# Kernel tuning notes

Hardware: AMD Instinct MI355X
Metric: run time of the kernel (lower is better)

## Reference

```python
import jax, jax.numpy as jnp
import numpy as np

BATCH, SEQ, HIDDEN = 2, 4096, 4096
HEADS, HEAD_DIM, BLOCK = 32, 128, 256
LAYER_IDX, N_LAYERS = 1, 32
EPS = 1e-5


def setup_inputs() -> dict:
    key = jax.random.key(0)
    ks = jax.random.split(key, 5)
    s = 0.02
    return {
        "hidden_states": jax.random.normal(ks[0], (BATCH, SEQ, HIDDEN), jnp.float32),
        "qkv_w": jax.random.normal(ks[1], (3 * HEADS * HEAD_DIM, HIDDEN), jnp.float32) * s,
        "out_w": jax.random.normal(ks[2], (HIDDEN, HEADS * HEAD_DIM), jnp.float32) * s,
        "gate_w": jax.random.normal(ks[3], (HEADS * HEAD_DIM, HIDDEN), jnp.float32) * s,
        "norm_w": jnp.ones((HEADS * HEAD_DIM,), jnp.float32),
    }


def _decays():
    # slope_rate: (h,1,1)
    base = 1.0 / 2.0 ** (8.0 / HEADS)
    exponent = jnp.arange(HEADS, dtype=jnp.float32) + 1.0
    factor = 1.0 - LAYER_IDX / (N_LAYERS - 1 + 1e-5) + 1e-5
    slope = (base ** exponent * factor)[:, None, None]
    r = jnp.arange(BLOCK, dtype=jnp.float32) + 1.0
    q_decay = jnp.exp(-slope * r[:, None])                 # (h, block, 1)
    k_decay = jnp.exp(-slope * (BLOCK - r)[:, None])       # (h, block, 1)
    diff = r[:, None] - r[None, :]                         # (block, block): i - j
    diag = slope[None] * diff[None, None]                  # (1, h, block, block)
    diag = jnp.where(diag >= 0, -diag, -jnp.inf)
    diag_decay = jnp.exp(diag)                             # causal intra-block decay
    block_decay = jnp.exp(-slope * BLOCK)                  # (h,1,1)
    return q_decay, k_decay, diag_decay, block_decay


def reference(hidden_states, qkv_w, out_w, gate_w, norm_w):
    b, s, _ = hidden_states.shape
    h, d, bs = HEADS, HEAD_DIM, BLOCK
    nb = s // bs
    q_decay, k_decay, diag_decay, block_decay = _decays()

    # qkv projection + silu, split per-head into q,k,v
    qkv = jax.nn.silu(hidden_states @ qkv_w.T)             # (b,s,3hd)
    qkv = qkv.reshape(b, s, h, 3, d)
    q = jnp.moveaxis(qkv[:, :, :, 0], 2, 1)                # (b,h,s,d)
    k = jnp.moveaxis(qkv[:, :, :, 1], 2, 1)
    v = jnp.moveaxis(qkv[:, :, :, 2], 2, 1)

    # split sequence into blocks, scan leading axis = block index
    def to_blocks(x):
        return jnp.moveaxis(x.reshape(b, h, nb, bs, d), 2, 0)  # (nb,b,h,bs,d)

    qb, kb, vb = to_blocks(q), to_blocks(k), to_blocks(v)

    def step(kv, blk):
        cq, ck, cv = blk
        # intra-block quadratic attention with causal decay
        scores = jnp.einsum('bhnd,bhmd->bhnm', cq, ck) * diag_decay
        intra = jnp.einsum('bhnm,bhmd->bhnd', scores, cv)
        # inter-block via decayed recurrent state kv: (b,h,d,d)
        inter = jnp.einsum('bhnd,bhde->bhne', cq * q_decay, kv)
        kv_next = kv * block_decay + jnp.einsum('bhnd,bhne->bhde', ck * k_decay, cv)
        return kv_next, intra + inter

    kv0 = jnp.zeros((b, h, d, d), hidden_states.dtype)
    _, out_blocks = jax.lax.scan(step, kv0, (qb, kb, vb))  # (nb,b,h,bs,d)

    attn = jnp.moveaxis(out_blocks, 0, 2)                  # (b,h,nb,bs,d)
    attn = attn.reshape(b, h, s, d).transpose(0, 2, 1, 3).reshape(b, s, h * d)

    # RMSNorm (fp32 accumulation, as MixtralRMSNorm)
    xf = attn.astype(jnp.float32)
    xf = xf * jax.lax.rsqrt(jnp.mean(xf * xf, axis=-1, keepdims=True) + EPS)
    normed = norm_w * xf.astype(attn.dtype)

    gate = jax.nn.sigmoid(hidden_states @ gate_w.T)
    return (gate * normed) @ out_w.T
```

## Files before the change

### kernel.cpp

```cpp
#include <hip/hip_runtime.h>

typedef unsigned short u16;
typedef __attribute__((ext_vector_type(4))) float f32x4;
typedef __attribute__((ext_vector_type(8))) __bf16 bf16x8;

#define SEQ   4096
#define HID   4096
#define HID3  12288

__device__ __forceinline__ float bf2f(u16 u){
  union { unsigned int i; float f; } v; v.i = ((unsigned int)u) << 16; return v.f;
}
__device__ __forceinline__ u16 f2bf(float f){
  union { float f; unsigned int i; } v; v.f = f;
  unsigned int r = (v.i + 0x7FFFu + ((v.i >> 16) & 1u)) >> 16;
  return (u16)r;
}
__device__ __forceinline__ float slope_of(int h){
  const float factor = 1.0f - 1.0f/(31.0f + 1e-5f) + 1e-5f;
  return exp2f(-0.25f * (float)(h + 1)) * factor;
}
__device__ __forceinline__ bf16x8 ld_bf8(const u16* p){
  return __builtin_bit_cast(bf16x8, *(const uint4*)p);
}
__device__ __forceinline__ void gload_lds16(const u16* g, u16* l){
  __builtin_amdgcn_global_load_lds((const __attribute__((address_space(1))) void*)g,
                                   (__attribute__((address_space(3))) void*)l, 16, 0, 0);
}

__global__ __launch_bounds__(256) void cvt4p_kernel(const float* __restrict__ s0,
                                                    const float* __restrict__ s1,
                                                    const float* __restrict__ s2,
                                                    const float* __restrict__ s3,
                                                    u16* __restrict__ dst){
  int c = blockIdx.x;
  int tr = c >> 7, kch = c & 127;
  const float* src; int rowbase;
  if (tr < 32){ src = s0; rowbase = tr * 256; }
  else if (tr < 80){ src = s1; rowbase = (tr - 32) * 256; }
  else if (tr < 96){ src = s2; rowbase = (tr - 80) * 256; }
  else { src = s3; rowbase = (tr - 96) * 256; }
  u16* out = dst + (long)c * 8192;
#pragma unroll
  for (int pass = 0; pass < 4; ++pass){
    int q = pass * 256 + threadIdx.x;
    int dr = q >> 3, up = q & 7;
    int ul = up ^ (dr & 7);
    int row = 2 * dr + (ul >> 2);
    int k8 = ul & 3;
    const float* sp = src + (long)(rowbase + row) * 4096 + kch * 32 + k8 * 8;
    float4 v0 = *(const float4*)sp;
    float4 v1 = *(const float4*)(sp + 4);
    ushort4 o0 = { f2bf(v0.x), f2bf(v0.y), f2bf(v0.z), f2bf(v0.w) };
    ushort4 o1 = { f2bf(v1.x), f2bf(v1.y), f2bf(v1.z), f2bf(v1.w) };
    *(ushort4*)(out + q * 8) = o0;
    *(ushort4*)(out + q * 8 + 4) = o1;
  }
}

template<int EPI>
__global__ __launch_bounds__(512) void gemm256(
    const u16* __restrict__ A, const u16* __restrict__ B, void* __restrict__ C,
    const u16* __restrict__ Aux, const float* __restrict__ Rs,
    const float* __restrict__ Nw, int M, int N, int K)
{
  __shared__ u16 ring[5][16384];
  const int t = threadIdx.x;
  const int w = t >> 6, l = t & 63, lr = l & 15, lk = l >> 4;
  const int mw = w >> 2, nw = w & 3;
  const int nbn = N >> 8;
  const int nkc = K >> 5;
  int nwg = gridDim.x;
  int bid = blockIdx.x;
  int bswz = (bid & 7) * (nwg >> 3) + (bid >> 3);
  int bm = bswz / nbn, bn = bswz % nbn;
  const int NT = K >> 6;

  int offA[8], offB[4];
#pragma unroll
  for (int fn = 0; fn < 8; ++fn){
    int row = mw * 128 + fn * 16 + lr;
    offA[fn] = (row >> 1) * 64 + (((((row & 1) << 2) + lk) ^ ((row >> 1) & 7)) << 3);
  }
#pragma unroll
  for (int fe = 0; fe < 4; ++fe){
    int row = nw * 64 + fe * 16 + lr;
    offB[fe] = (row >> 1) * 64 + (((((row & 1) << 2) + lk) ^ ((row >> 1) & 7)) << 3);
  }

  auto stageA = [&](int kt, int c, int slot, int i){
    gload_lds16(A + ((long)bm * nkc + kt * 2 + c) * 8192 + i * 4096 + t * 8,
                &ring[slot][i * 4096 + w * 512]);
  };
  auto stageB = [&](int kt, int c, int slot, int i){
    gload_lds16(B + ((long)bn * nkc + kt * 2 + c) * 8192 + i * 4096 + t * 8,
                &ring[slot][8192 + i * 4096 + w * 512]);
  };

  f32x4 acc[8][4] = {};

  stageA(0,0,0,0); stageA(0,0,0,1); stageB(0,0,0,0); stageB(0,0,0,1);
  stageA(0,1,1,0); stageA(0,1,1,1); stageB(0,1,1,0); stageB(0,1,1,1);
  if (1 < NT){ stageA(1,0,2,0); stageA(1,0,2,1); stageB(1,0,2,0); stageB(1,0,2,1); }
  asm volatile("s_waitcnt vmcnt(4)" ::: "memory");
  __builtin_amdgcn_s_barrier();

  int sa = 0;
  for (int p = 0; p < NT; ++p){
    int sb = sa + 1; if (sb >= 5) sb -= 5;
    int sx = sa + 3; if (sx >= 5) sx -= 5;
    int sy = sa + 4; if (sy >= 5) sy -= 5;
    const u16* Aa = &ring[sa][0];
    const u16* Ab = &ring[sb][0];
    const u16* Ba = &ring[sa][8192];
    const u16* Bb = &ring[sb][8192];
    bf16x8 bh0[4], bh1[4], afc0[8], afc1[8];

#pragma unroll
    for (int fe = 0; fe < 4; ++fe) bh0[fe] = ld_bf8(Ba + offB[fe]);
#pragma unroll
    for (int fn = 0; fn < 4; ++fn) afc0[fn] = ld_bf8(Aa + offA[fn]);
#pragma unroll
    for (int fn = 4; fn < 8; ++fn) afc0[fn] = ld_bf8(Aa + offA[fn]);
    if (p + 1 < NT){ stageA(p+1, 1, sx, 0); stageA(p+1, 1, sx, 1); }
    asm volatile("s_waitcnt lgkmcnt(4)" ::: "memory");
    __builtin_amdgcn_sched_barrier(0);
    __builtin_amdgcn_s_setprio(1);
#pragma unroll
    for (int fn = 0; fn < 4; ++fn)
#pragma unroll
      for (int fe = 0; fe < 4; ++fe)
        acc[fn][fe] = __builtin_amdgcn_mfma_f32_16x16x32_bf16(afc0[fn], bh0[fe], acc[fn][fe], 0, 0, 0);
    __builtin_amdgcn_s_setprio(0);

#pragma unroll
    for (int fe = 0; fe < 4; ++fe) bh1[fe] = ld_bf8(Bb + offB[fe]);
#pragma unroll
    for (int fn = 0; fn < 4; ++fn) afc1[fn] = ld_bf8(Ab + offA[fn]);
    if (p + 1 < NT){ stageB(p+1, 1, sx, 0); stageB(p+1, 1, sx, 1); }
    asm volatile("s_waitcnt lgkmcnt(8)" ::: "memory");
    __builtin_amdgcn_sched_barrier(0);
    __builtin_amdgcn_s_setprio(1);
#pragma unroll
    for (int fn = 4; fn < 8; ++fn)
#pragma unroll
      for (int fe = 0; fe < 4; ++fe)
        acc[fn][fe] = __builtin_amdgcn_mfma_f32_16x16x32_bf16(afc0[fn], bh0[fe], acc[fn][fe], 0, 0, 0);
    __builtin_amdgcn_s_setprio(0);

#pragma unroll
    for (int fn = 4; fn < 8; ++fn) afc1[fn] = ld_bf8(Ab + offA[fn]);
    if (p + 2 < NT){ stageA(p+2, 0, sy, 0); stageA(p+2, 0, sy, 1); }
    asm volatile("s_waitcnt lgkmcnt(4)" ::: "memory");
    __builtin_amdgcn_sched_barrier(0);
    __builtin_amdgcn_s_setprio(1);
#pragma unroll
    for (int fn = 0; fn < 4; ++fn)
#pragma unroll
      for (int fe = 0; fe < 4; ++fe)
        acc[fn][fe] = __builtin_amdgcn_mfma_f32_16x16x32_bf16(afc1[fn], bh1[fe], acc[fn][fe], 0, 0, 0);
    __builtin_amdgcn_s_setprio(0);

    if (p + 2 < NT){ stageB(p+2, 0, sy, 0); stageB(p+2, 0, sy, 1); }
    asm volatile("s_waitcnt lgkmcnt(0)" ::: "memory");
    __builtin_amdgcn_sched_barrier(0);
    __builtin_amdgcn_s_setprio(1);
#pragma unroll
    for (int fn = 4; fn < 8; ++fn)
#pragma unroll
      for (int fe = 0; fe < 4; ++fe)
        acc[fn][fe] = __builtin_amdgcn_mfma_f32_16x16x32_bf16(afc1[fn], bh1[fe], acc[fn][fe], 0, 0, 0);
    __builtin_amdgcn_s_setprio(0);

    if (p + 2 < NT) asm volatile("s_waitcnt vmcnt(4)" ::: "memory");
    else            asm volatile("s_waitcnt vmcnt(0)" ::: "memory");
    __builtin_amdgcn_s_barrier();
    sa += 2; if (sa >= 5) sa -= 5;
  }

  long crow = (long)bm * 256 + mw * 128 + lk * 4;
  long ccol = (long)bn * 256 + nw * 64 + lr;
#pragma unroll
  for (int fn = 0; fn < 8; ++fn)
#pragma unroll
    for (int fe = 0; fe < 4; ++fe)
#pragma unroll
      for (int reg = 0; reg < 4; ++reg){
        long row = crow + fn * 16 + reg;
        long col = ccol + fe * 16;
        float x = acc[fn][fe][reg];
        if (EPI == 0){
          ((u16*)C)[row * N + col] = f2bf(x / (1.0f + __expf(-x)));
        } else if (EPI == 1){
          float g = 1.0f / (1.0f + __expf(-x));
          float a = bf2f(Aux[row * N + col]);
          int r256 = (int)row & 255;
          int dr2 = r256 >> 1;
          int ul2 = ((r256 & 1) << 2) | (((int)col & 31) >> 3);
          int u2 = ul2 ^ (dr2 & 7);
          long idx = ((long)(row >> 8) * 128 + (col >> 5)) * 8192 + dr2 * 64 + u2 * 8 + (col & 7);
          ((u16*)C)[idx] = f2bf(g * a * Rs[row] * Nw[col]);
        } else {
          ((float*)C)[row * N + col] = x;
        }
      }
}

__global__ __launch_bounds__(256) void attn_contrib(
    const u16* __restrict__ qkv, float* __restrict__ ct)
{
  __shared__ u16 VT[128 * 258];
  __shared__ u16 KT[128 * 258];
  int wg = blockIdx.x;
  int bh = wg >> 4, blk = wg & 15;
  int b = bh >> 5, h = bh & 31;
  int t = threadIdx.x;
  float slope = slope_of(h);
  const u16* kg = qkv + ((long)(b * SEQ + blk * 256)) * HID3 + h * 384 + 128;
  const u16* vg = kg + 128;
#pragma unroll
  for (int i = 0; i < 16; ++i){
    int chunk = t + i * 256;
    int row = chunk >> 4, c8 = (chunk & 15) << 3;
    float kd = __expf(-slope * (float)(255 - row));
    uint4 kk = *(const uint4*)&kg[(long)row * HID3 + c8];
    uint4 vv = *(const uint4*)&vg[(long)row * HID3 + c8];
    const u16* ks = (const u16*)&kk;
    const u16* vs = (const u16*)&vv;
#pragma unroll
    for (int x = 0; x < 8; ++x){
      KT[(c8 + x) * 258 + row] = f2bf(bf2f(ks[x]) * kd);
      VT[(c8 + x) * 258 + row] = vs[x];
    }
  }
  __syncthreads();
  int w = t >> 6, l = t & 63, lr = l & 15, lk = l >> 4;
  int we = (w >> 1) * 64, wd = (w & 1) * 64;
  f32x4 acc[4][4] = {};
  for (int nc = 0; nc < 8; ++nc){
    bf16x8 va[4], kb[4];
#pragma unroll
    for (int f = 0; f < 4; ++f) va[f] = ld_bf8(&VT[(we + f * 16 + lr) * 258 + nc * 32 + lk * 8]);
#pragma unroll
    for (int f = 0; f < 4; ++f) kb[f] = ld_bf8(&KT[(wd + f * 16 + lr) * 258 + nc * 32 + lk * 8]);
#pragma unroll
    for (int fe = 0; fe < 4; ++fe)
#pragma unroll
      for (int fd = 0; fd < 4; ++fd)
        acc[fe][fd] = __builtin_amdgcn_mfma_f32_16x16x32_bf16(va[fe], kb[fd], acc[fe][fd], 0, 0, 0);
  }
  float* out = ct + (long)wg * 16384;
#pragma unroll
  for (int fe = 0; fe < 4; ++fe)
#pragma unroll
    for (int fd = 0; fd < 4; ++fd)
#pragma unroll
      for (int reg = 0; reg < 4; ++reg){
        int e = we + fe * 16 + lk * 4 + reg;
        int d = wd + fd * 16 + lr;
        out[e * 128 + d] = acc[fe][fd][reg];
      }
}

__global__ __launch_bounds__(256) void attn_scan(const float* __restrict__ ct,
                                                 u16* __restrict__ stTb)
{
  int g = blockIdx.x;
  int bh = g >> 2, sl = g & 3;
  int t = threadIdx.x;
  float bdec = __expf(-slope_of(bh & 31) * 256.0f);
  float cur[16];
#pragma unroll
  for (int i = 0; i < 16; ++i) cur[i] = 0.f;
  const float* base = ct + (long)bh * 16 * 16384 + sl * 4096;
  u16* ob = stTb + (long)bh * 16 * 16384 + sl * 4096;
  for (int blkI = 0; blkI < 16; ++blkI){
    const float* p = base + (long)blkI * 16384;
    u16* o = ob + (long)blkI * 16384;
#pragma unroll
    for (int i = 0; i < 16; ++i){
      o[t + i * 256] = f2bf(cur[i]);
      cur[i] = cur[i] * bdec + p[t + i * 256];
    }
  }
}

__global__ __launch_bounds__(512) void attn_mfma(
    const u16* __restrict__ qkv, const u16* __restrict__ stTb, u16* __restrict__ attn)
{
  __shared__ u16 Ks[256 * 130];
  __shared__ u16 VTs[128 * 258];
  __shared__ u16 Ps[4][64 * 34];
  int wg = blockIdx.x;
  int bh = wg >> 4, blk = wg & 15;
  int b = bh >> 5, h = bh & 31;
  int t = threadIdx.x;
  int w = t >> 6, l = t & 63, lr = l & 15, lk = l >> 4;
  int r = w >> 1, c = w & 1;
  float slope = slope_of(h);
  const u16* qg = qkv + ((long)(b * SEQ + blk * 256)) * HID3 + h * 384;
  const u16* kg = qg + 128;
  const u16* vg = qg + 256;

#pragma unroll
  for (int i = 0; i < 8; ++i){
    int chunk = t + i * 512;
    int row = chunk >> 4, c8 = (chunk & 15) << 3;
    *(uint4*)&Ks[row * 130 + c8] = *(const uint4*)&kg[(long)row * HID3 + c8];
    uint4 vv = *(const uint4*)&vg[(long)row * HID3 + c8];
    const u16* vs = (const u16*)&vv;
#pragma unroll
    for (int x = 0; x < 8; ++x) VTs[(c8 + x) * 258 + row] = vs[x];
  }
  bf16x8 qa[4][4];
#pragma unroll
  for (int fn = 0; fn < 4; ++fn)
#pragma unroll
    for (int kc = 0; kc < 4; ++kc)
      qa[fn][kc] = ld_bf8(&qg[(long)(r * 64 + fn * 16 + lr) * HID3 + kc * 32 + lk * 8]);
  f32x4 acc[4][4] = {};
  __syncthreads();

  int mtmax = 2 * r + 1;
  for (int mt = 0; mt < 8; ++mt){
    if (mt <= mtmax){
      f32x4 S[4] = {};
      int mrow = mt * 32 + c * 16 + lr;
      bf16x8 kb[4];
#pragma unroll
      for (int kc = 0; kc < 4; ++kc)
        kb[kc] = ld_bf8(&Ks[mrow * 130 + kc * 32 + lk * 8]);
#pragma unroll
      for (int fn = 0; fn < 4; ++fn)
#pragma unroll
        for (int kc = 0; kc < 4; ++kc)
          S[fn] = __builtin_amdgcn_mfma_f32_16x16x32_bf16(qa[fn][kc], kb[kc], S[fn], 0, 0, 0);
      int m = mt * 32 + c * 16 + lr;
#pragma unroll
      for (int fn = 0; fn < 4; ++fn)
#pragma unroll
        for (int reg = 0; reg < 4; ++reg){
          int n = r * 64 + fn * 16 + lk * 4 + reg;
          float dv = (n >= m) ? __expf(-slope * (float)(n - m)) : 0.f;
          Ps[r][(fn * 16 + lk * 4 + reg) * 34 + c * 16 + lr] = f2bf(S[fn][reg] * dv);
        }
    }
    __syncthreads();
    if (mt <= mtmax){
      bf16x8 pa[4], vb[4];
#pragma unroll
      for (int fn = 0; fn < 4; ++fn)
        pa[fn] = ld_bf8(&Ps[r][(fn * 16 + lr) * 34 + lk * 8]);
#pragma unroll
      for (int fe = 0; fe < 4; ++fe)
        vb[fe] = ld_bf8(&VTs[(c * 64 + fe * 16 + lr) * 258 + mt * 32 + lk * 8]);
#pragma unroll
      for (int fn = 0; fn < 4; ++fn)
#pragma unroll
        for (int fe = 0; fe < 4; ++fe)
          acc[fn][fe] = __builtin_amdgcn_mfma_f32_16x16x32_bf16(pa[fn], vb[fe], acc[fn][fe], 0, 0, 0);
    }
    __syncthreads();
  }

#pragma unroll
  for (int fn = 0; fn < 4; ++fn){
    int n = r * 64 + fn * 16 + lr;
    float qd = __expf(-slope * (float)(n + 1));
#pragma unroll
    for (int kc = 0; kc < 4; ++kc){
      union { bf16x8 v; u16 u[8]; } uu; uu.v = qa[fn][kc];
#pragma unroll
      for (int x = 0; x < 8; ++x) uu.u[x] = f2bf(bf2f(uu.u[x]) * qd);
      qa[fn][kc] = uu.v;
    }
  }
  const u16* sg = stTb + (long)(bh * 16 + blk) * 16384;
#pragma unroll
  for (int kc = 0; kc < 4; ++kc){
    bf16x8 sb2[4];
#pragma unroll
    for (int fe = 0; fe < 4; ++fe)
      sb2[fe] = ld_bf8(&sg[(c * 64 + fe * 16 + lr) * 128 + kc * 32 + lk * 8]);
#pragma unroll
    for (int fn = 0; fn < 4; ++fn)
#pragma unroll
      for (int fe = 0; fe < 4; ++fe)
        acc[fn][fe] = __builtin_amdgcn_mfma_f32_16x16x32_bf16(qa[fn][kc], sb2[fe], acc[fn][fe], 0, 0, 0);
  }

  u16* arow = attn + ((long)(b * SEQ + blk * 256)) * HID + h * 128;
#pragma unroll
  for (int fn = 0; fn < 4; ++fn)
#pragma unroll
    for (int fe = 0; fe < 4; ++fe)
#pragma unroll
      for (int reg = 0; reg < 4; ++reg){
        int n = r * 64 + fn * 16 + lk * 4 + reg;
        int col = c * 64 + fe * 16 + lr;
        arow[(long)n * HID + col] = f2bf(acc[fn][fe][reg]);
      }
}

__global__ __launch_bounds__(256) void rmsnorm_stats(const u16* __restrict__ attn,
                                                     float* __restrict__ rs)
{
  __shared__ float wsum[4];
  int row = blockIdx.x, t = threadIdx.x;
  const u16* p = attn + (long)row * HID;
  uint4 v0 = *(const uint4*)&p[t * 8];
  uint4 v1 = *(const uint4*)&p[t * 8 + 2048];
  const u16* a0 = (const u16*)&v0;
  const u16* a1 = (const u16*)&v1;
  float ss = 0.f;
#pragma unroll
  for (int x = 0; x < 8; ++x){
    float f0 = bf2f(a0[x]), f1 = bf2f(a1[x]);
    ss += f0 * f0 + f1 * f1;
  }
#pragma unroll
  for (int off = 32; off > 0; off >>= 1) ss += __shfl_down(ss, off);
  if ((t & 63) == 0) wsum[t >> 6] = ss;
  __syncthreads();
  if (t == 0)
    rs[row] = rsqrtf((wsum[0] + wsum[1] + wsum[2] + wsum[3]) * (1.0f / 4096.0f) + 1e-5f);
}

extern "C" void kernel_launch(void* const* d_in, const int* in_sizes, int n_in,
                              void* d_out, int out_size, void* d_ws, size_t ws_size,
                              hipStream_t stream)
{
  const float* hidden = (const float*)d_in[0];
  const float* qkv_w  = (const float*)d_in[1];
  const float* out_w  = (const float*)d_in[2];
  const float* gate_w = (const float*)d_in[3];
  const float* norm_w = (const float*)d_in[4];
  char* ws = (char*)d_ws;
  const long SZ_X  = 67108864L;
  const long SZ_WQ = 100663296L;
  const long SZ_WG = 33554432L;
  const long SZ_WO = 33554432L;
  const long SZ_QA = 201326592L;
  const long SZ_AT = 67108864L;
  u16* Xb   = (u16*)(ws);
  u16* Wq   = (u16*)(ws + SZ_X);
  u16* Wg   = (u16*)(ws + SZ_X + SZ_WQ);
  u16* Wo   = (u16*)(ws + SZ_X + SZ_WQ + SZ_WG);
  u16* qact = (u16*)(ws + SZ_X + SZ_WQ + SZ_WG + SZ_WO);
  u16* attn = (u16*)(ws + SZ_X + SZ_WQ + SZ_WG + SZ_WO + SZ_QA);
  float* st   = (float*)Wq;
  u16*   stTb = (u16*)(ws + SZ_X + 67108864L);
  float* rsbuf = (float*)Wq;
  u16* gated = qact;
  if (ws_size < (size_t)(SZ_X + SZ_WQ + SZ_WG + SZ_WO + SZ_QA + SZ_AT)) return;

  cvt4p_kernel<<<14336, 256, 0, stream>>>(hidden, qkv_w, gate_w, out_w, Xb);

  gemm256<0><<<32 * 48, 512, 0, stream>>>(Xb, Wq, (void*)qact, nullptr, nullptr, nullptr,
                                          8192, 12288, 4096);

  attn_contrib<<<1024, 256, 0, stream>>>(qact, st);
  attn_scan<<<256, 256, 0, stream>>>(st, stTb);
  attn_mfma<<<1024, 512, 0, stream>>>(qact, stTb, attn);
  rmsnorm_stats<<<8192, 256, 0, stream>>>(attn, rsbuf);

  gemm256<1><<<32 * 16, 512, 0, stream>>>(Xb, Wg, (void*)gated, attn, rsbuf, norm_w,
                                          8192, 4096, 4096);
  gemm256<2><<<32 * 16, 512, 0, stream>>>(gated, Wo, d_out, nullptr, nullptr, nullptr,
                                          8192, 4096, 4096);
}
```

Measured before the change: 1.529 ms.

## Load GEMM B operand directly from global into double-buffered registers, skipping LDS

The B tile is no longer staged through the shared-memory ring. Each wave now loads its B fragments straight from the pre-packed global layout into two register buffers, which alternate between even and odd iterations. This halves LDS use, which could allow a second workgroup per CU, and removes the LDS writes and reads for B. In exchange it raises register pressure, repeats B global reads across the waves that share a column slice, and relies on the vmcnt accounting and an even iteration count staying correct.

```diff
diff --git a/kernel.cpp b/kernel.cpp
--- a/kernel.cpp
+++ b/kernel.cpp
@@ -64,7 +64,7 @@
     const u16* __restrict__ Aux, const float* __restrict__ Rs,
     const float* __restrict__ Nw, int M, int N, int K)
 {
-  __shared__ u16 ring[5][16384];
+  __shared__ u16 ring[5][8192];
   const int t = threadIdx.x;
   const int w = t >> 6, l = t & 63, lr = l & 15, lk = l >> 4;
   const int mw = w >> 2, nw = w & 3;
@@ -92,36 +92,38 @@
     gload_lds16(A + ((long)bm * nkc + kt * 2 + c) * 8192 + i * 4096 + t * 8,
                 &ring[slot][i * 4096 + w * 512]);
   };
-  auto stageB = [&](int kt, int c, int slot, int i){
-    gload_lds16(B + ((long)bn * nkc + kt * 2 + c) * 8192 + i * 4096 + t * 8,
-                &ring[slot][8192 + i * 4096 + w * 512]);
+  const u16* Bt = B + (long)bn * nkc * 8192;
+  auto loadB = [&](int kt, bf16x8 (&dst)[4][2]){
+#pragma unroll
+    for (int c = 0; c < 2; ++c){
+      const u16* bc = Bt + ((long)kt * 2 + c) * 8192;
+#pragma unroll
+      for (int fe = 0; fe < 4; ++fe) dst[fe][c] = ld_bf8(bc + offB[fe]);
+    }
   };
 
   f32x4 acc[8][4] = {};
-
-  stageA(0,0,0,0); stageA(0,0,0,1); stageB(0,0,0,0); stageB(0,0,0,1);
-  stageA(0,1,1,0); stageA(0,1,1,1); stageB(0,1,1,0); stageB(0,1,1,1);
-  if (1 < NT){ stageA(1,0,2,0); stageA(1,0,2,1); stageB(1,0,2,0); stageB(1,0,2,1); }
-  asm volatile("s_waitcnt vmcnt(4)" ::: "memory");
+  bf16x8 bX[4][2], bY[4][2];
+
+  loadB(0, bX);
+  stageA(0,0,0,0); stageA(0,0,0,1);
+  stageA(0,1,1,0); stageA(0,1,1,1);
+  stageA(1,0,2,0); stageA(1,0,2,1);
+  asm volatile("s_waitcnt vmcnt(2)" ::: "memory");
   __builtin_amdgcn_s_barrier();
 
   int sa = 0;
-  for (int p = 0; p < NT; ++p){
+  auto period = [&](int p, bf16x8 (&bcur)[4][2], bf16x8 (&bnext)[4][2]){
     int sb = sa + 1; if (sb >= 5) sb -= 5;
     int sx = sa + 3; if (sx >= 5) sx -= 5;
     int sy = sa + 4; if (sy >= 5) sy -= 5;
     const u16* Aa = &ring[sa][0];
     const u16* Ab = &ring[sb][0];
-    const u16* Ba = &ring[sa][8192];
-    const u16* Bb = &ring[sb][8192];
-    bf16x8 bh0[4], bh1[4], afc0[8], afc1[8];
-
-#pragma unroll
-    for (int fe = 0; fe < 4; ++fe) bh0[fe] = ld_bf8(Ba + offB[fe]);
-#pragma unroll
-    for (int fn = 0; fn < 4; ++fn) afc0[fn] = ld_bf8(Aa + offA[fn]);
-#pragma unroll
-    for (int fn = 4; fn < 8; ++fn) afc0[fn] = ld_bf8(Aa + offA[fn]);
+    bf16x8 afc0[8], afc1[8];
+
+    if (p + 1 < NT) loadB(p + 1, bnext);
+#pragma unroll
+    for (int fn = 0; fn < 8; ++fn) afc0[fn] = ld_bf8(Aa + offA[fn]);
     if (p + 1 < NT){ stageA(p+1, 1, sx, 0); stageA(p+1, 1, sx, 1); }
     asm volatile("s_waitcnt lgkmcnt(4)" ::: "memory");
     __builtin_amdgcn_sched_barrier(0);
@@ -130,22 +132,19 @@
     for (int fn = 0; fn < 4; ++fn)
 #pragma unroll
       for (int fe = 0; fe < 4; ++fe)
-        acc[fn][fe] = __builtin_amdgcn_mfma_f32_16x16x32_bf16(afc0[fn], bh0[fe], acc[fn][fe], 0, 0, 0);
+        acc[fn][fe] = __builtin_amdgcn_mfma_f32_16x16x32_bf16(afc0[fn], bcur[fe][0], acc[fn][fe], 0, 0, 0);
     __builtin_amdgcn_s_setprio(0);
 
 #pragma unroll
-    for (int fe = 0; fe < 4; ++fe) bh1[fe] = ld_bf8(Bb + offB[fe]);
-#pragma unroll
     for (int fn = 0; fn < 4; ++fn) afc1[fn] = ld_bf8(Ab + offA[fn]);
-    if (p + 1 < NT){ stageB(p+1, 1, sx, 0); stageB(p+1, 1, sx, 1); }
-    asm volatile("s_waitcnt lgkmcnt(8)" ::: "memory");
+    asm volatile("s_waitcnt lgkmcnt(4)" ::: "memory");
     __builtin_amdgcn_sched_barrier(0);
     __builtin_amdgcn_s_setprio(1);
 #pragma unroll
     for (int fn = 4; fn < 8; ++fn)
 #pragma unroll
       for (int fe = 0; fe < 4; ++fe)
-        acc[fn][fe] = __builtin_amdgcn_mfma_f32_16x16x32_bf16(afc0[fn], bh0[fe], acc[fn][fe], 0, 0, 0);
+        acc[fn][fe] = __builtin_amdgcn_mfma_f32_16x16x32_bf16(afc0[fn], bcur[fe][0], acc[fn][fe], 0, 0, 0);
     __builtin_amdgcn_s_setprio(0);
 
 #pragma unroll
@@ -158,10 +157,9 @@
     for (int fn = 0; fn < 4; ++fn)
 #pragma unroll
       for (int fe = 0; fe < 4; ++fe)
-        acc[fn][fe] = __builtin_amdgcn_mfma_f32_16x16x32_bf16(afc1[fn], bh1[fe], acc[fn][fe], 0, 0, 0);
+        acc[fn][fe] = __builtin_amdgcn_mfma_f32_16x16x32_bf16(afc1[fn], bcur[fe][1], acc[fn][fe], 0, 0, 0);
     __builtin_amdgcn_s_setprio(0);
 
-    if (p + 2 < NT){ stageB(p+2, 0, sy, 0); stageB(p+2, 0, sy, 1); }
     asm volatile("s_waitcnt lgkmcnt(0)" ::: "memory");
     __builtin_amdgcn_sched_barrier(0);
     __builtin_amdgcn_s_setprio(1);
@@ -169,13 +167,18 @@
     for (int fn = 4; fn < 8; ++fn)
 #pragma unroll
       for (int fe = 0; fe < 4; ++fe)
-        acc[fn][fe] = __builtin_amdgcn_mfma_f32_16x16x32_bf16(afc1[fn], bh1[fe], acc[fn][fe], 0, 0, 0);
+        acc[fn][fe] = __builtin_amdgcn_mfma_f32_16x16x32_bf16(afc1[fn], bcur[fe][1], acc[fn][fe], 0, 0, 0);
     __builtin_amdgcn_s_setprio(0);
 
-    if (p + 2 < NT) asm volatile("s_waitcnt vmcnt(4)" ::: "memory");
+    if (p + 2 < NT) asm volatile("s_waitcnt vmcnt(2)" ::: "memory");
     else            asm volatile("s_waitcnt vmcnt(0)" ::: "memory");
     __builtin_amdgcn_s_barrier();
     sa += 2; if (sa >= 5) sa -= 5;
+  };
+
+  for (int p = 0; p < NT; p += 2){
+    period(p,     bX, bY);
+    period(p + 1, bY, bX);
   }
 
   long crow = (long)bm * 256 + mw * 128 + lk * 4;
```

Result: slower. 3.447 ms (+125.4%).
